# Optimization experiments

Measured on AMD Instinct MI355X. Metric: run time of the kernel, lower is better.

The kernel has to match this reference:

```python
import jax, jax.numpy as jnp
import numpy as np

MICRO_BATCHES = 4
NUM_EXPERTS = 8  # world_size=1 -> num_local_experts = 8
EPS = 1e-5


def setup_inputs() -> dict:
    key = jax.random.key(0)
    ks = jax.random.split(key, 8)
    B, S, D = 8, 2048, 1024
    E, F = NUM_EXPERTS, 4 * D
    x = jax.random.normal(ks[0], (B, S, D), dtype=jnp.float32)
    gamma = jnp.ones((D,), jnp.float32)
    beta = jnp.zeros((D,), jnp.float32)
    gate_w = jax.random.normal(ks[1], (E, D), jnp.float32) * (1.0 / np.sqrt(D))
    w1 = jax.random.normal(ks[2], (E, D, F), jnp.float32) * (1.0 / np.sqrt(D))
    b1 = jnp.zeros((E, F), jnp.float32)
    w2 = jax.random.normal(ks[3], (E, F, D), jnp.float32) * (1.0 / np.sqrt(F))
    b2 = jnp.zeros((E, D), jnp.float32)
    return {"x": x, "gamma": gamma, "beta": beta, "gate_w": gate_w,
            "w1": w1, "b1": b1, "w2": w2, "b2": b2}


def reference(x, gamma, beta, gate_w, w1, b1, w2, b2):
    B, S, D = x.shape
    E = w1.shape[0]
    # micro-batch chunking along batch dim (chunk(MICRO_BATCHES, dim=0))
    xf = x.reshape(MICRO_BATCHES, -1, D)            # [MB, T, D], T = B/MB * S
    T = xf.shape[1]
    # residual (gated_input) is the pre-LN flat input
    # moe_norm: LayerNorm over last dim, biased variance, eps=1e-5
    mu = jnp.mean(xf, axis=-1, keepdims=True)
    var = jnp.mean(jnp.square(xf - mu), axis=-1, keepdims=True)
    xn = (xf - mu) * jax.lax.rsqrt(var + EPS) * gamma + beta  # [MB, T, D]
    # gate logits + topk are computed in the source but discarded
    _logits = jnp.einsum('mtd,ed->mte', xn, gate_w)
    _ = jax.lax.top_k(_logits, 2)
    # dispatch/combine are identity for world_size=1; tokens split round-robin
    # into num_local_experts contiguous chunks per micro-batch
    tpe = T // E
    xe = xn.reshape(MICRO_BATCHES, E, tpe, D)       # [MB, E, tpe, D]
    h = jax.nn.gelu(jnp.einsum('metd,edf->metf', xe, w1) + b1[None, :, None, :],
                    approximate=False)
    y = jnp.einsum('metf,efd->metd', h, w2) + b2[None, :, None, :]
    out = xf + y.reshape(MICRO_BATCHES, T, D)       # residual add
    return out.reshape(B, S, D)
```

## Files before the change

kernel.cpp:

```cpp
#include <hip/hip_runtime.h>
#include <stdint.h>
#include <math.h>

typedef unsigned short ushort_t;
typedef __attribute__((ext_vector_type(8))) short bf16x8;
typedef __attribute__((ext_vector_type(4))) float f32x4;

#define SLOT 32768
#define EPI_STRIDE 1032

__device__ __forceinline__ ushort_t f2bf(float f) {
  union { float f; unsigned u; } cv; cv.f = f;
  unsigned r = cv.u + 0x7fffu + ((cv.u >> 16) & 1u);
  return (ushort_t)(r >> 16);
}

__device__ __forceinline__ void gl_lds16(const void* g, void* l) {
  typedef __attribute__((address_space(1))) const char gchar;
  typedef __attribute__((address_space(3))) char lchar;
  __builtin_amdgcn_global_load_lds((gchar*)g, (lchar*)l, 16, 0, 0);
}

__device__ __forceinline__ f32x4 MFMA(bf16x8 a, bf16x8 b, f32x4 c) {
  return __builtin_amdgcn_mfma_f32_16x16x32_bf16(a, b, c, 0, 0, 0);
}

__global__ __launch_bounds__(256) void ln_kernel(const float* __restrict__ x,
                                                 const float* __restrict__ gamma,
                                                 const float* __restrict__ beta,
                                                 ushort_t* __restrict__ xn) {
  const int row = blockIdx.x;
  const int t = threadIdx.x;
  const float4 v = ((const float4*)(x + (size_t)row * 1024))[t];
  float s  = v.x + v.y + v.z + v.w;
  float ss = v.x * v.x + v.y * v.y + v.z * v.z + v.w * v.w;
#pragma unroll
  for (int o = 32; o >= 1; o >>= 1) {
    s  += __shfl_xor(s, o);
    ss += __shfl_xor(ss, o);
  }
  __shared__ float red[10];
  const int wave = t >> 6, lane = t & 63;
  if (lane == 0) { red[wave] = s; red[4 + wave] = ss; }
  __syncthreads();
  if (t == 0) {
    float S  = red[0] + red[1] + red[2] + red[3];
    float SS = red[4] + red[5] + red[6] + red[7];
    float mu  = S * (1.0f / 1024.0f);
    float var = SS * (1.0f / 1024.0f) - mu * mu;
    red[8] = mu;
    red[9] = rsqrtf(var + 1e-5f);
  }
  __syncthreads();
  const float mu = red[8], rs = red[9];
  const float4 g = ((const float4*)gamma)[t];
  const float4 b = ((const float4*)beta)[t];
  ushort4 o;
  o.x = f2bf((v.x - mu) * rs * g.x + b.x);
  o.y = f2bf((v.y - mu) * rs * g.y + b.y);
  o.z = f2bf((v.z - mu) * rs * g.z + b.z);
  o.w = f2bf((v.w - mu) * rs * g.w + b.w);
  ((ushort4*)(xn + (size_t)row * 1024))[t] = o;
}

__global__ __launch_bounds__(256) void transpose_cast(const float* __restrict__ in,
                                                      ushort_t* __restrict__ out,
                                                      int R, int C) {
  __shared__ float tile[32][33];
  const int e = blockIdx.z;
  const float* src = in + (size_t)e * R * C;
  ushort_t* dst = out + (size_t)e * R * C;
  const int c0 = blockIdx.x * 32, r0 = blockIdx.y * 32;
  const int tx = threadIdx.x, ty = threadIdx.y;
#pragma unroll
  for (int j = 0; j < 32; j += 8)
    tile[ty + j][tx] = src[(size_t)(r0 + ty + j) * C + c0 + tx];
  __syncthreads();
#pragma unroll
  for (int j = 0; j < 32; j += 8)
    dst[(size_t)(c0 + ty + j) * R + r0 + tx] = f2bf(tile[tx][ty + j]);
}


__device__ __forceinline__ void stage_half(const ushort_t* gsrc, int lda,
                                           char* half_base, int kt, int tid) {
  const int rr = tid >> 2;
  const int gs = (tid & 3) ^ ((tid >> 3) & 3);
  gl_lds16(gsrc + (size_t)rr * lda + kt + gs * 8, half_base + (tid >> 6) * 1024);
}

template <int BASE>
__device__ __forceinline__ void mfma16(const bf16x8 (&a)[4], const bf16x8 (&b)[4],
                                       f32x4 (&acc)[8][4]) {
  __builtin_amdgcn_s_setprio(1);
#pragma unroll
  for (int mi = 0; mi < 4; mi++)
#pragma unroll
    for (int ni = 0; ni < 4; ni++)
      acc[BASE + mi][ni] = MFMA(a[mi], b[ni], acc[BASE + mi][ni]);
  __builtin_amdgcn_s_setprio(0);
}

template <int VM, bool STG, bool LAST>
__device__ __forceinline__ void tile_body(char* smem, int T,
                                          const ushort_t* gA, const ushort_t* gB,
                                          int lda, int a_off, int b_off, int tid,
                                          bf16x8 (&bA0)[4], bf16x8 (&bA1)[4],
                                          bf16x8 (&bBc)[4], bf16x8 (&bBn)[4],
                                          f32x4 (&acc)[8][4]) {
  const char* slot = smem + (T & 3) * SLOT;
  char* nstg = smem + ((T + 3) & 3) * SLOT;
  const int kt3 = (T + 3) * 32;
#pragma unroll
  for (int mi = 0; mi < 4; mi++) bA1[mi] = *(const bf16x8*)(slot + a_off + (mi + 4) * 1024);
  if (STG) {
    stage_half(gA, lda, nstg, kt3, tid);
    stage_half(gA + (size_t)128 * lda, lda, nstg + 8192, kt3, tid);
  }
  __builtin_amdgcn_sched_barrier(0);
  __builtin_amdgcn_s_barrier();
  __builtin_amdgcn_sched_barrier(0);
  mfma16<0>(bA0, bBc, acc);
  __builtin_amdgcn_s_barrier();
  if (VM == 6)      asm volatile("s_waitcnt vmcnt(6)" ::: "memory");
  else if (VM == 4) asm volatile("s_waitcnt vmcnt(4)" ::: "memory");
  else if (VM == 0) asm volatile("s_waitcnt vmcnt(0)" ::: "memory");
  __builtin_amdgcn_s_barrier();
  if (!LAST) {
    const char* nslot = smem + ((T + 1) & 3) * SLOT;
#pragma unroll
    for (int ni = 0; ni < 4; ni++) bBn[ni] = *(const bf16x8*)(nslot + b_off + ni * 1024);
#pragma unroll
    for (int mi = 0; mi < 4; mi++) bA0[mi] = *(const bf16x8*)(nslot + a_off + mi * 1024);
    if (STG) {
      stage_half(gB, lda, nstg + 16384, kt3, tid);
      stage_half(gB + (size_t)128 * lda, lda, nstg + 24576, kt3, tid);
    }
  }
  __builtin_amdgcn_sched_barrier(0);
  mfma16<4>(bA1, bBc, acc);
  __builtin_amdgcn_s_barrier();
}

template <int EPI, int LDA, int LDC, int KTOT>
__global__ __launch_bounds__(512, 2) void gemm256(const ushort_t* __restrict__ A,
                                                  const ushort_t* __restrict__ Bw,
                                                  const float* __restrict__ bias,
                                                  const float* __restrict__ resid,
                                                  ushort_t* __restrict__ Hout,
                                                  float* __restrict__ Fout) {
  extern __shared__ char smem[];
  const int tid = threadIdx.x;
  const int wave = tid >> 6, lane = tid & 63;

  const int bid = blockIdx.x;
  const int c = bid & 7, l = bid >> 3;
  const int tm = c * 8 + (l & 7);
  const int tn = l >> 3;
  const int row0 = tm * 256;
  const int col0 = tn * 256;
  const int e = (row0 >> 9) & 7;

  const ushort_t* gA = A + (size_t)row0 * LDA;
  const ushort_t* gB = Bw + ((size_t)e * LDC + col0) * LDA;

  const int NT = KTOT / 32;

  const int wm = wave >> 2, wn = wave & 3;
  const int l15 = lane & 15, g = lane >> 4;
  const int sw = ((g ^ ((lane >> 1) & 3)) << 4);
  const int a_off = wm * 8192 + l15 * 64 + sw;
  const int b_off = 16384 + (wn >> 1) * 8192 + (wn & 1) * 4096 + l15 * 64 + sw;

  f32x4 acc[8][4] = {};
  bf16x8 bA0[4], bA1[4], bB0[4], bB1[4];

#pragma unroll
  for (int T = 0; T < 3; ++T) {
    char* s = smem + T * SLOT;
    stage_half(gA, LDA, s, T * 32, tid);
    stage_half(gA + (size_t)128 * LDA, LDA, s + 8192, T * 32, tid);
    stage_half(gB, LDA, s + 16384, T * 32, tid);
    stage_half(gB + (size_t)128 * LDA, LDA, s + 24576, T * 32, tid);
  }
  asm volatile("s_waitcnt vmcnt(8)" ::: "memory");
  __builtin_amdgcn_s_barrier();
#pragma unroll
  for (int ni = 0; ni < 4; ni++) bB0[ni] = *(const bf16x8*)(smem + b_off + ni * 1024);
#pragma unroll
  for (int mi = 0; mi < 4; mi++) bA0[mi] = *(const bf16x8*)(smem + a_off + mi * 1024);

  for (int T = 0; T < NT - 4; T += 2) {
    tile_body<6, true, false>(smem, T,     gA, gB, LDA, a_off, b_off, tid, bA0, bA1, bB0, bB1, acc);
    tile_body<6, true, false>(smem, T + 1, gA, gB, LDA, a_off, b_off, tid, bA0, bA1, bB1, bB0, acc);
  }
  tile_body<6, true,  false>(smem, NT - 4, gA, gB, LDA, a_off, b_off, tid, bA0, bA1, bB0, bB1, acc);
  tile_body<4, false, false>(smem, NT - 3, gA, gB, LDA, a_off, b_off, tid, bA0, bA1, bB1, bB0, acc);
  tile_body<0, false, false>(smem, NT - 2, gA, gB, LDA, a_off, b_off, tid, bA0, bA1, bB0, bB1, acc);
  tile_body<-1, false, true>(smem, NT - 1, gA, gB, LDA, a_off, b_off, tid, bA0, bA1, bB1, bB0, acc);

  __syncthreads();

  float bv[4];
#pragma unroll
  for (int ni = 0; ni < 4; ni++)
    bv[ni] = bias[e * LDC + col0 + wn * 64 + ni * 16 + l15];

#pragma unroll
  for (int r = 0; r < 4; ++r) {
#pragma unroll
    for (int mh = 0; mh < 2; ++mh) {
      const int mi = 2 * r + mh;
      const int lrow = wm * 32 + mh * 16 + g * 4;
#pragma unroll
      for (int ni = 0; ni < 4; ++ni) {
        const int colb = (wn * 64 + ni * 16 + l15) * 4;
#pragma unroll
        for (int rr = 0; rr < 4; ++rr) {
          float v = acc[mi][ni][rr] + bv[ni];
          if (EPI == 0) {
            float v2 = v * v;
            float cc = fmaf(0.044715f, v2, 1.0f);
            float u  = exp2f(-2.3022078f * v * cc);
            v = __fdividef(v, 1.0f + u);
          }
          *(float*)(smem + (size_t)(lrow + rr) * EPI_STRIDE + colb) = v;
        }
      }
    }
    __syncthreads();
#pragma unroll
    for (int i = 0; i < 8; ++i) {
      const int chunk = i * 512 + tid;
      const int lr = chunk >> 6;
      const int cb = (chunk & 63) * 16;
      const float4 v4 = *(const float4*)(smem + (size_t)lr * EPI_STRIDE + cb);
      const int grow = row0 + (lr < 32 ? r * 32 + lr : 128 + r * 32 + (lr - 32));
      const int gcol = col0 + (chunk & 63) * 4;
      if (EPI == 0) {
        ushort4 o;
        o.x = f2bf(v4.x); o.y = f2bf(v4.y); o.z = f2bf(v4.z); o.w = f2bf(v4.w);
        *(ushort4*)(&Hout[(size_t)grow * LDC + gcol]) = o;
      } else {
        const float4 rs = *(const float4*)(&resid[(size_t)grow * LDC + gcol]);
        float4 o;
        o.x = v4.x + rs.x; o.y = v4.y + rs.y; o.z = v4.z + rs.z; o.w = v4.w + rs.w;
        *(float4*)(&Fout[(size_t)grow * LDC + gcol]) = o;
      }
    }
    __syncthreads();
  }
}

extern "C" void kernel_launch(void* const* d_in, const int* in_sizes, int n_in,
                              void* d_out, int out_size, void* d_ws, size_t ws_size,
                              hipStream_t stream) {
  const float* x     = (const float*)d_in[0];
  const float* gamma = (const float*)d_in[1];
  const float* beta  = (const float*)d_in[2];
  const float* w1    = (const float*)d_in[4];
  const float* b1    = (const float*)d_in[5];
  const float* w2    = (const float*)d_in[6];
  const float* b2    = (const float*)d_in[7];
  float* out = (float*)d_out;

  char* ws = (char*)d_ws;
  ushort_t* xn  = (ushort_t*)ws;
  ushort_t* w1t = (ushort_t*)(ws + 33554432);
  ushort_t* w2t = (ushort_t*)(ws + 33554432 + 67108864);
  ushort_t* h   = (ushort_t*)(ws + 33554432 + 2 * 67108864);

  hipFuncSetAttribute(reinterpret_cast<const void*>(&gemm256<0, 1024, 4096, 1024>),
                      hipFuncAttributeMaxDynamicSharedMemorySize, 131072);
  hipFuncSetAttribute(reinterpret_cast<const void*>(&gemm256<1, 4096, 1024, 4096>),
                      hipFuncAttributeMaxDynamicSharedMemorySize, 131072);

  ln_kernel<<<16384, 256, 0, stream>>>(x, gamma, beta, xn);
  transpose_cast<<<dim3(128, 32, 8), dim3(32, 8), 0, stream>>>(w1, w1t, 1024, 4096);
  transpose_cast<<<dim3(32, 128, 8), dim3(32, 8), 0, stream>>>(w2, w2t, 4096, 1024);

  gemm256<0, 1024, 4096, 1024><<<dim3(1024), 512, 131072, stream>>>(xn, w1t, b1, nullptr, h, nullptr);
  gemm256<1, 4096, 1024, 4096><<<dim3(256), 512, 131072, stream>>>(h, w2t, b2, x, nullptr, out);
}
```

Measured before the change: 424.0 us.

## Restructure GEMM mainloop to double-buffered 64-wide K tiles with inline ds_read

Replaces the four-slot, K=32 pipeline with a two-set double buffer holding 64-wide K tiles (128-byte rows, XOR swizzle over 8 groups). Each tile is consumed in four MFMA phases that re-read A fragments while B fragments stay in registers, using inline ds_read_b128 with immediate offsets. The aim is fewer barriers and address computations per K step and more MFMAs per LDS round. The trade-off is a shallower prefetch depth, since each group waits on vmcnt(0), plus more LDS per block, which may expose global-load latency.

```diff
diff --git a/kernel.cpp b/kernel.cpp
--- a/kernel.cpp
+++ b/kernel.cpp
@@ -6,8 +6,13 @@
 typedef __attribute__((ext_vector_type(8))) short bf16x8;
 typedef __attribute__((ext_vector_type(4))) float f32x4;
 
-#define SLOT 32768
 #define EPI_STRIDE 1032
+
+#define DS_READ(D, B, O) asm volatile("ds_read_b128 %0, %1 offset:" O : "=v"(D) : "v"(B))
+#define SCHED0 __builtin_amdgcn_sched_barrier(0)
+#define BAR __builtin_amdgcn_s_barrier()
+#define WAITL0 asm volatile("s_waitcnt lgkmcnt(0)" ::: "memory")
+#define WAITV0 asm volatile("s_waitcnt vmcnt(0)" ::: "memory")
 
 __device__ __forceinline__ ushort_t f2bf(float f) {
   union { float f; unsigned u; } cv; cv.f = f;
@@ -19,6 +24,11 @@
   typedef __attribute__((address_space(1))) const char gchar;
   typedef __attribute__((address_space(3))) char lchar;
   __builtin_amdgcn_global_load_lds((gchar*)g, (lchar*)l, 16, 0, 0);
+}
+
+__device__ __forceinline__ unsigned lds_addr(void* p) {
+  typedef __attribute__((address_space(3))) char lchar;
+  return (unsigned)(unsigned long long)(lchar*)p;
 }
 
 __device__ __forceinline__ f32x4 MFMA(bf16x8 a, bf16x8 b, f32x4 c) {
@@ -82,64 +92,64 @@
 }
 
 
-__device__ __forceinline__ void stage_half(const ushort_t* gsrc, int lda,
-                                           char* half_base, int kt, int tid) {
-  const int rr = tid >> 2;
-  const int gs = (tid & 3) ^ ((tid >> 3) & 3);
-  gl_lds16(gsrc + (size_t)rr * lda + kt + gs * 8, half_base + (tid >> 6) * 1024);
-}
-
-template <int BASE>
-__device__ __forceinline__ void mfma16(const bf16x8 (&a)[4], const bf16x8 (&b)[4],
+template <int Q>
+__device__ __forceinline__ void mfma_phase(const bf16x8& a00, const bf16x8& a01,
+                                           const bf16x8& a10, const bf16x8& a11,
+                                           bf16x8 (&b0)[4], bf16x8 (&b1)[4],
+                                           f32x4 (&acc)[8][4]) {
+  __builtin_amdgcn_s_setprio(1);
+#pragma unroll
+  for (int n = 0; n < 4; n++) acc[2*Q+0][n] = MFMA(a00, b0[n], acc[2*Q+0][n]);
+#pragma unroll
+  for (int n = 0; n < 4; n++) acc[2*Q+1][n] = MFMA(a01, b0[n], acc[2*Q+1][n]);
+#pragma unroll
+  for (int n = 0; n < 4; n++) acc[2*Q+0][n] = MFMA(a10, b1[n], acc[2*Q+0][n]);
+#pragma unroll
+  for (int n = 0; n < 4; n++) acc[2*Q+1][n] = MFMA(a11, b1[n], acc[2*Q+1][n]);
+  __builtin_amdgcn_s_setprio(0);
+}
+
+template <bool STG, int LDA>
+__device__ __forceinline__ void group4(unsigned aG0, unsigned aG1,
+                                       unsigned bG0, unsigned bG1,
+                                       const ushort_t* sA, const ushort_t* sB,
+                                       int kt, char* dstSet, int wave,
                                        f32x4 (&acc)[8][4]) {
-  __builtin_amdgcn_s_setprio(1);
-#pragma unroll
-  for (int mi = 0; mi < 4; mi++)
-#pragma unroll
-    for (int ni = 0; ni < 4; ni++)
-      acc[BASE + mi][ni] = MFMA(a[mi], b[ni], acc[BASE + mi][ni]);
-  __builtin_amdgcn_s_setprio(0);
-}
-
-template <int VM, bool STG, bool LAST>
-__device__ __forceinline__ void tile_body(char* smem, int T,
-                                          const ushort_t* gA, const ushort_t* gB,
-                                          int lda, int a_off, int b_off, int tid,
-                                          bf16x8 (&bA0)[4], bf16x8 (&bA1)[4],
-                                          bf16x8 (&bBc)[4], bf16x8 (&bBn)[4],
-                                          f32x4 (&acc)[8][4]) {
-  const char* slot = smem + (T & 3) * SLOT;
-  char* nstg = smem + ((T + 3) & 3) * SLOT;
-  const int kt3 = (T + 3) * 32;
-#pragma unroll
-  for (int mi = 0; mi < 4; mi++) bA1[mi] = *(const bf16x8*)(slot + a_off + (mi + 4) * 1024);
+  bf16x8 b0[4], b1[4], a00, a01, a10, a11;
+  DS_READ(b0[0], bG0, "0");    DS_READ(b0[1], bG0, "2048");
+  DS_READ(b0[2], bG0, "4096"); DS_READ(b0[3], bG0, "6144");
+  DS_READ(b1[0], bG1, "0");    DS_READ(b1[1], bG1, "2048");
+  DS_READ(b1[2], bG1, "4096"); DS_READ(b1[3], bG1, "6144");
+  DS_READ(a00, aG0, "0");      DS_READ(a01, aG0, "2048");
+  DS_READ(a10, aG1, "0");      DS_READ(a11, aG1, "2048");
   if (STG) {
-    stage_half(gA, lda, nstg, kt3, tid);
-    stage_half(gA + (size_t)128 * lda, lda, nstg + 8192, kt3, tid);
-  }
-  __builtin_amdgcn_sched_barrier(0);
-  __builtin_amdgcn_s_barrier();
-  __builtin_amdgcn_sched_barrier(0);
-  mfma16<0>(bA0, bBc, acc);
-  __builtin_amdgcn_s_barrier();
-  if (VM == 6)      asm volatile("s_waitcnt vmcnt(6)" ::: "memory");
-  else if (VM == 4) asm volatile("s_waitcnt vmcnt(4)" ::: "memory");
-  else if (VM == 0) asm volatile("s_waitcnt vmcnt(0)" ::: "memory");
-  __builtin_amdgcn_s_barrier();
-  if (!LAST) {
-    const char* nslot = smem + ((T + 1) & 3) * SLOT;
-#pragma unroll
-    for (int ni = 0; ni < 4; ni++) bBn[ni] = *(const bf16x8*)(nslot + b_off + ni * 1024);
-#pragma unroll
-    for (int mi = 0; mi < 4; mi++) bA0[mi] = *(const bf16x8*)(nslot + a_off + mi * 1024);
-    if (STG) {
-      stage_half(gB, lda, nstg + 16384, kt3, tid);
-      stage_half(gB + (size_t)128 * lda, lda, nstg + 24576, kt3, tid);
-    }
-  }
-  __builtin_amdgcn_sched_barrier(0);
-  mfma16<4>(bA1, bBc, acc);
-  __builtin_amdgcn_s_barrier();
+    char* dA = dstSet + wave * 1024;
+    char* dB = dstSet + 32768 + wave * 1024;
+#pragma unroll
+    for (int c2 = 0; c2 < 4; ++c2)
+      gl_lds16(sA + (size_t)c2 * 64 * LDA + kt, dA + c2 * 8192);
+#pragma unroll
+    for (int c2 = 0; c2 < 4; ++c2)
+      gl_lds16(sB + (size_t)c2 * 64 * LDA + kt, dB + c2 * 8192);
+  }
+  SCHED0; BAR; WAITL0; SCHED0;
+  mfma_phase<0>(a00, a01, a10, a11, b0, b1, acc);
+  SCHED0; BAR;
+  DS_READ(a00, aG0, "4096"); DS_READ(a01, aG0, "6144");
+  DS_READ(a10, aG1, "4096"); DS_READ(a11, aG1, "6144");
+  SCHED0; BAR; WAITL0; SCHED0;
+  mfma_phase<1>(a00, a01, a10, a11, b0, b1, acc);
+  SCHED0; BAR;
+  DS_READ(a00, aG0, "8192"); DS_READ(a01, aG0, "10240");
+  DS_READ(a10, aG1, "8192"); DS_READ(a11, aG1, "10240");
+  SCHED0; BAR; WAITL0; SCHED0;
+  mfma_phase<2>(a00, a01, a10, a11, b0, b1, acc);
+  SCHED0; BAR;
+  DS_READ(a00, aG0, "12288"); DS_READ(a01, aG0, "14336");
+  DS_READ(a10, aG1, "12288"); DS_READ(a11, aG1, "14336");
+  SCHED0; BAR; WAITL0; SCHED0;
+  mfma_phase<3>(a00, a01, a10, a11, b0, b1, acc);
+  SCHED0; WAITV0; BAR; SCHED0;
 }
 
 template <int EPI, int LDA, int LDC, int KTOT>
@@ -164,40 +174,46 @@
   const ushort_t* gA = A + (size_t)row0 * LDA;
   const ushort_t* gB = Bw + ((size_t)e * LDC + col0) * LDA;
 
-  const int NT = KTOT / 32;
+  const int NI = KTOT / 128;
 
   const int wm = wave >> 2, wn = wave & 3;
-  const int l15 = lane & 15, g = lane >> 4;
-  const int sw = ((g ^ ((lane >> 1) & 3)) << 4);
-  const int a_off = wm * 8192 + l15 * 64 + sw;
-  const int b_off = 16384 + (wn >> 1) * 8192 + (wn & 1) * 4096 + l15 * 64 + sw;
+  const int l15 = lane & 15, g = lane >> 4, l7 = lane & 7;
+
+  const unsigned lds0 = lds_addr(smem);
+  const unsigned g0 = ((unsigned)((g     ) ^ l7)) << 4;
+  const unsigned g1 = ((unsigned)((g + 4 ) ^ l7)) << 4;
+  const unsigned aS0g0 = lds0 + (wm * 128 + l15) * 128 + g0;
+  const unsigned aS0g1 = lds0 + (wm * 128 + l15) * 128 + g1;
+  const unsigned bS0g0 = lds0 + 32768 + (wn * 64 + l15) * 128 + g0;
+  const unsigned bS0g1 = lds0 + 32768 + (wn * 64 + l15) * 128 + g1;
+  const unsigned aS1g0 = aS0g0 + 65536, aS1g1 = aS0g1 + 65536;
+  const unsigned bS1g0 = bS0g0 + 65536, bS1g1 = bS0g1 + 65536;
+
+  const int sgr = (tid & 7) ^ ((tid >> 3) & 7);
+  const ushort_t* sA = gA + (size_t)(tid >> 3) * LDA + sgr * 8;
+  const ushort_t* sB = gB + (size_t)(tid >> 3) * LDA + sgr * 8;
 
   f32x4 acc[8][4] = {};
-  bf16x8 bA0[4], bA1[4], bB0[4], bB1[4];
-
-#pragma unroll
-  for (int T = 0; T < 3; ++T) {
-    char* s = smem + T * SLOT;
-    stage_half(gA, LDA, s, T * 32, tid);
-    stage_half(gA + (size_t)128 * LDA, LDA, s + 8192, T * 32, tid);
-    stage_half(gB, LDA, s + 16384, T * 32, tid);
-    stage_half(gB + (size_t)128 * LDA, LDA, s + 24576, T * 32, tid);
-  }
-  asm volatile("s_waitcnt vmcnt(8)" ::: "memory");
-  __builtin_amdgcn_s_barrier();
-#pragma unroll
-  for (int ni = 0; ni < 4; ni++) bB0[ni] = *(const bf16x8*)(smem + b_off + ni * 1024);
-#pragma unroll
-  for (int mi = 0; mi < 4; mi++) bA0[mi] = *(const bf16x8*)(smem + a_off + mi * 1024);
-
-  for (int T = 0; T < NT - 4; T += 2) {
-    tile_body<6, true, false>(smem, T,     gA, gB, LDA, a_off, b_off, tid, bA0, bA1, bB0, bB1, acc);
-    tile_body<6, true, false>(smem, T + 1, gA, gB, LDA, a_off, b_off, tid, bA0, bA1, bB1, bB0, acc);
-  }
-  tile_body<6, true,  false>(smem, NT - 4, gA, gB, LDA, a_off, b_off, tid, bA0, bA1, bB0, bB1, acc);
-  tile_body<4, false, false>(smem, NT - 3, gA, gB, LDA, a_off, b_off, tid, bA0, bA1, bB1, bB0, acc);
-  tile_body<0, false, false>(smem, NT - 2, gA, gB, LDA, a_off, b_off, tid, bA0, bA1, bB0, bB1, acc);
-  tile_body<-1, false, true>(smem, NT - 1, gA, gB, LDA, a_off, b_off, tid, bA0, bA1, bB1, bB0, acc);
+
+  {
+    char* dA = smem + wave * 1024;
+    char* dB = smem + 32768 + wave * 1024;
+#pragma unroll
+    for (int c2 = 0; c2 < 4; ++c2)
+      gl_lds16(sA + (size_t)c2 * 64 * LDA, dA + c2 * 8192);
+#pragma unroll
+    for (int c2 = 0; c2 < 4; ++c2)
+      gl_lds16(sB + (size_t)c2 * 64 * LDA, dB + c2 * 8192);
+  }
+  WAITV0; BAR; SCHED0;
+
+#pragma unroll 1
+  for (int i = 0; i < NI - 1; ++i) {
+    group4<true, LDA>(aS0g0, aS0g1, bS0g0, bS0g1, sA, sB, (2*i+1)*64, smem + 65536, wave, acc);
+    group4<true, LDA>(aS1g0, aS1g1, bS1g0, bS1g1, sA, sB, (2*i+2)*64, smem,         wave, acc);
+  }
+  group4<true,  LDA>(aS0g0, aS0g1, bS0g0, bS0g1, sA, sB, (2*NI-1)*64, smem + 65536, wave, acc);
+  group4<false, LDA>(aS1g0, aS1g1, bS1g0, bS1g1, sA, sB, 0,           smem,         wave, acc);
 
   __syncthreads();
 
```

New measurement: 431.0 us. Within noise of the previous version (+1.7%).
